# Performance work log

Hardware: AMD Instinct MI355X
Metric: run time of the kernel (lower is better)

The kernel has to match this reference:

```python
import jax, jax.numpy as jnp
import numpy as np

NI = 256        # in_channels
QK = NI // 8    # query/key channels = 32
BS, H, W = 4, 64, 64


def setup_inputs() -> dict:
    key = jax.random.key(0)
    ks = jax.random.split(key, 8)
    x = jax.random.normal(ks[0], (BS, NI, H, W), dtype=jnp.float32)
    # 1x1 conv weights stored as [out_ch, in_ch] (kernel is 1x1)
    wq = jax.random.normal(ks[1], (QK, NI), dtype=jnp.float32) * (1.0 / np.sqrt(NI))
    bq = jnp.zeros((QK,), dtype=jnp.float32)
    wk = jax.random.normal(ks[2], (QK, NI), dtype=jnp.float32) * (1.0 / np.sqrt(NI))
    bk = jnp.zeros((QK,), dtype=jnp.float32)
    wv = jax.random.normal(ks[3], (NI, NI), dtype=jnp.float32) * (1.0 / np.sqrt(NI))
    bv = jnp.zeros((NI,), dtype=jnp.float32)
    # gamma is zero-init in the module; use small random values so the
    # attention branch actually contributes (post-training state).
    gamma = jax.random.normal(ks[4], (1, NI, 1, 1), dtype=jnp.float32) * 0.1
    return {"x": x, "wq": wq, "bq": bq, "wk": wk, "bk": bk,
            "wv": wv, "bv": bv, "gamma": gamma}


def reference(x, wq, bq, wk, bk, wv, bv, gamma):
    bs, c, h, w = x.shape
    n = h * w
    xf = x.reshape(bs, c, n)                       # [bs, c, N]
    # 1x1 convs == per-pixel linear maps over channels
    q = jnp.einsum('oc,bcn->bno', wq, xf) + bq     # [bs, N, qk]
    k = jnp.einsum('oc,bcn->bon', wk, xf) + bk[None, :, None]  # [bs, qk, N]
    v = jnp.einsum('oc,bcn->bon', wv, xf) + bv[None, :, None]  # [bs, c, N]
    attn = jax.nn.softmax(jnp.einsum('bnq,bqm->bnm', q, k), axis=-1)  # [bs, N, N]
    out = jnp.einsum('bcm,bnm->bcn', v, attn)      # value @ attn^T
    out = out.reshape(bs, c, h, w)
    return gamma * out + x
```

## Files before the change

### kernel.cpp

```cpp
#include <hip/hip_runtime.h>
#include <cstdint>
#include <cstddef>

#define NI   256
#define QKC  32
#define BS   4
#define NPIX 4096
#define LOG2E 1.4426950408889634f

typedef __bf16 bf16x8 __attribute__((ext_vector_type(8)));
typedef __bf16 bf16x4 __attribute__((ext_vector_type(4)));
typedef float  f32x16 __attribute__((ext_vector_type(16)));

__device__ inline f32x16 zero16() {
    f32x16 z;
    #pragma unroll
    for (int i = 0; i < 16; ++i) z[i] = 0.f;
    return z;
}

__global__ __launch_bounds__(256) void wconv_pack(
    const float* __restrict__ wq, const float* __restrict__ wk,
    const float* __restrict__ wv, __bf16* __restrict__ wpk)
{
    int f = blockIdx.x * 256 + threadIdx.x;
    int otl = f >> 10, rem = f & 1023;
    int kk = rem >> 6, h = (rem >> 5) & 1, l31 = rem & 31;
    int och = otl * 32 + l31, c0 = kk * 16 + 8 * h;
    const float* src = och < 32 ? wq + och * NI + c0
                     : och < 64 ? wk + (och - 32) * NI + c0
                                : wv + (och - 64) * NI + c0;
    float4 x0 = *(const float4*)src;
    float4 x1 = *(const float4*)(src + 4);
    __align__(16) __bf16 o8[8] = {
        (__bf16)x0.x, (__bf16)x0.y, (__bf16)x0.z, (__bf16)x0.w,
        (__bf16)x1.x, (__bf16)x1.y, (__bf16)x1.z, (__bf16)x1.w};
    *(uint4*)(wpk + (size_t)f * 8) = *(const uint4*)o8;
}

__global__ __launch_bounds__(256) void qkv_mfma(
    const float* __restrict__ x, const __bf16* __restrict__ wpk,
    const float* __restrict__ bq, const float* __restrict__ bk,
    const float* __restrict__ bv,
    __bf16* __restrict__ qpk, __bf16* __restrict__ kpk, __bf16* __restrict__ vpk)
{
    __shared__ __align__(16) __bf16 xT[32][264];
    __shared__ float bls[320];

    const int t = threadIdx.x, w = t >> 6, lane = t & 63;
    const int l31 = lane & 31, h = lane >> 5;
    const int b = blockIdx.y, n0 = blockIdx.x * 32, kt = blockIdx.x;

    for (int i = t; i < 320; i += 256)
        bls[i] = i < 32 ? bq[i] : i < 64 ? bk[i - 32] : bv[i - 64];

    {
        int n4 = (t & 7) * 4, cb = (t >> 3) * 8;
        float4 xv[8];
        #pragma unroll
        for (int j = 0; j < 8; ++j)
            xv[j] = *(const float4*)(x + ((size_t)(b * NI) + cb + j) * NPIX + n0 + n4);
        #pragma unroll
        for (int i = 0; i < 4; ++i) {
            __align__(16) __bf16 r8[8];
            #pragma unroll
            for (int j = 0; j < 8; ++j) r8[j] = (__bf16)((&xv[j].x)[i]);
            *(uint4*)&xT[n4 + i][cb] = *(const uint4*)r8;
        }
    }
    __syncthreads();

    f32x16 acc[3] = {zero16(), zero16(), zero16()};
    #pragma unroll 4
    for (int kk = 0; kk < 16; ++kk) {
        bf16x8 xf = *(const bf16x8*)&xT[l31][kk * 16 + 8 * h];
        #pragma unroll
        for (int jj = 0; jj < 3; ++jj) {
            int otl = w + 4 * jj;
            if (otl < 10) {
                bf16x8 wf = *(const bf16x8*)(wpk + (size_t)((otl * 16 + kk) * 64 + 32 * h + l31) * 8);
                acc[jj] = __builtin_amdgcn_mfma_f32_32x32x16_bf16(wf, xf, acc[jj], 0, 0, 0);
            }
        }
    }
    __syncthreads();

    __bf16 (*vT)[264] = xT;
    #pragma unroll
    for (int jj = 0; jj < 3; ++jj) {
        int otl = w + 4 * jj;
        if (otl >= 2 && otl < 10) {
            #pragma unroll
            for (int qd = 0; qd < 4; ++qd) {
                int c0v = (otl - 2) * 32 + 8 * qd + 4 * h;
                __align__(8) __bf16 q4[4];
                #pragma unroll
                for (int i = 0; i < 4; ++i)
                    q4[i] = (__bf16)(acc[jj][4 * qd + i] + bls[64 + c0v + i]);
                *(uint2*)&vT[l31][c0v] = *(const uint2*)q4;
            }
        }
    }
    #pragma unroll
    for (int jj = 0; jj < 3; ++jj) {
        int otl = w + 4 * jj;
        if (otl == 0) {
            #pragma unroll
            for (int kc = 0; kc < 2; ++kc) {
                __align__(16) __bf16 hi8[8], lo8[8];
                #pragma unroll
                for (int j = 0; j < 8; ++j) {
                    int r = 8 * kc + j;
                    int och = (r & 3) + 8 * (r >> 2) + 4 * h;
                    float val = (acc[jj][r] + bls[och]) * LOG2E;
                    __bf16 hh = (__bf16)val;
                    hi8[j] = hh;
                    lo8[j] = (__bf16)(val - (float)hh);
                }
                size_t base = ((((size_t)(b * 128 + kt) * 2 + 0) * 2 + kc) * 2 + h) * 32 + l31;
                *(uint4*)(qpk + base * 8) = *(const uint4*)hi8;
                size_t basel = ((((size_t)(b * 128 + kt) * 2 + 1) * 2 + kc) * 2 + h) * 32 + l31;
                *(uint4*)(qpk + basel * 8) = *(const uint4*)lo8;
            }
        } else if (otl == 1) {
            #pragma unroll
            for (int kc = 0; kc < 2; ++kc) {
                __align__(16) __bf16 k8[8];
                #pragma unroll
                for (int j = 0; j < 8; ++j) {
                    int r = 8 * kc + j;
                    int och = (r & 3) + 8 * (r >> 2) + 4 * h;
                    k8[j] = (__bf16)(acc[jj][r] + bls[32 + och]);
                }
                size_t base = (((size_t)(b * 128 + kt) * 2 + kc) * 2 + h) * 32 + l31;
                *(uint4*)(kpk + base * 8) = *(const uint4*)k8;
            }
        }
    }
    __syncthreads();

    #pragma unroll
    for (int kc = 0; kc < 2; ++kc)
        #pragma unroll
        for (int hh = 0; hh < 2; ++hh) {
            __align__(16) __bf16 f8[8];
            #pragma unroll
            for (int j = 0; j < 8; ++j) f8[j] = vT[16 * kc + 8 * hh + j][t];
            size_t base = (((size_t)(b * 128 + kt) * 2 + kc) * 2 + hh) * 256 + t;
            *(uint4*)(vpk + base * 8) = *(const uint4*)f8;
        }
}

__global__ __launch_bounds__(256, 4) void attn_mfma(
    const __bf16* __restrict__ qpk, const __bf16* __restrict__ kpk,
    const __bf16* __restrict__ vpk,
    __bf16* __restrict__ Opart, float* __restrict__ dpart)
{
    constexpr int MT = 32;
    __shared__ __align__(16) __bf16 pt_s[2][64][72];
    __shared__ float dwave[4][32];

    const int t = threadIdx.x;
    const int b = blockIdx.z;
    const int ksp = blockIdx.y >> 1, cs = blockIdx.y & 1;
    const int n0 = blockIdx.x * 64;
    const int w = t >> 6, lane = t & 63, l31 = lane & 31, h = lane >> 5;
    const int sr = w & 1, sc = w >> 1;
    const int kt0 = ksp * 64;
    const int cbase = 128 * cs + 32 * w + l31;

    const int qt = 2 * blockIdx.x + sr;
    bf16x8 qf[2][2];
    #pragma unroll
    for (int hl = 0; hl < 2; ++hl)
        #pragma unroll
        for (int kc = 0; kc < 2; ++kc)
            qf[hl][kc] = *(const bf16x8*)(qpk +
                (((((size_t)(b * 128 + qt) * 2 + hl) * 2 + kc) * 2 + h) * 32 + l31) * 8);

    auto kload = [&](int ktile, int kc) {
        return *(const bf16x8*)(kpk +
            ((((size_t)(b * 128 + ktile) * 2 + kc) * 2 + h) * 32 + l31) * 8);
    };
    const __bf16* vbase = vpk +
        ((((size_t)(b * 128 + kt0) * 2) * 2 + h) * 256 + cbase) * 8;

    f32x16 a0 = zero16(), a1 = zero16();
    float dacc = 0.f;

    auto sblock = [&](bf16x8 kh0, bf16x8 kh1, int buf) {
        f32x16 s = zero16();
        __builtin_amdgcn_s_setprio(1);
        s = __builtin_amdgcn_mfma_f32_32x32x16_bf16(kh0, qf[0][0], s, 0, 0, 0);
        s = __builtin_amdgcn_mfma_f32_32x32x16_bf16(kh1, qf[0][1], s, 0, 0, 0);
        s = __builtin_amdgcn_mfma_f32_32x32x16_bf16(kh0, qf[1][0], s, 0, 0, 0);
        s = __builtin_amdgcn_mfma_f32_32x32x16_bf16(kh1, qf[1][1], s, 0, 0, 0);
        __builtin_amdgcn_s_setprio(0);
        #pragma unroll
        for (int qd = 0; qd < 4; ++qd) {
            __align__(8) __bf16 e4[4];
            #pragma unroll
            for (int i = 0; i < 4; ++i) {
                float e = __builtin_amdgcn_exp2f(s[4 * qd + i]);
                dacc += e;
                e4[i] = (__bf16)e;
            }
            *(uint2*)&pt_s[buf][32 * sr + l31][32 * sc + 8 * qd + 4 * h] = *(const uint2*)e4;
        }
    };

    bf16x8 kh0 = kload(kt0 + sc, 0), kh1 = kload(kt0 + sc, 1);
    sblock(kh0, kh1, 0);
    kh0 = kload(kt0 + 2 + sc, 0); kh1 = kload(kt0 + 2 + sc, 1);
    __syncthreads();

    for (int mt = 0; mt < MT; ++mt) {
        const int cur = mt & 1;

        bf16x8 vf[2][2];
        #pragma unroll
        for (int i = 0; i < 2; ++i)
            #pragma unroll
            for (int kc = 0; kc < 2; ++kc)
                vf[i][kc] = *(const bf16x8*)(vbase +
                    ((size_t)(2 * mt + i) * 2 + kc) * (2 * 256 * 8));

        if (mt < MT - 1) {
            bf16x8 k0 = kh0, k1 = kh1;
            if (mt < MT - 2) {
                kh0 = kload(kt0 + 2 * (mt + 2) + sc, 0);
                kh1 = kload(kt0 + 2 * (mt + 2) + sc, 1);
            }
            sblock(k0, k1, 1 - cur);
        }

        __builtin_amdgcn_s_setprio(1);
        #pragma unroll
        for (int i = 0; i < 2; ++i)
            #pragma unroll
            for (int kc = 0; kc < 2; ++kc) {
                int col = 32 * i + 16 * kc + 8 * h;
                bf16x8 pa0 = *(const bf16x8*)&pt_s[cur][l31][col];
                bf16x8 pa1 = *(const bf16x8*)&pt_s[cur][32 + l31][col];
                a0 = __builtin_amdgcn_mfma_f32_32x32x16_bf16(pa0, vf[i][kc], a0, 0, 0, 0);
                a1 = __builtin_amdgcn_mfma_f32_32x32x16_bf16(pa1, vf[i][kc], a1, 0, 0, 0);
            }
        __builtin_amdgcn_s_setprio(0);
        __syncthreads();
    }

    float dtot = dacc + __shfl_xor(dacc, 32);
    if (lane < 32) dwave[w][l31] = dtot;
    __syncthreads();
    if (cs == 0 && w < 2 && lane < 32) {
        size_t dbase = ((size_t)(ksp * BS + b)) * NPIX + n0 + 32 * w;
        dpart[dbase + l31] = dwave[w][l31] + dwave[w + 2][l31];
    }

    size_t obase = (((size_t)(ksp * BS + b)) * NI + cbase) * NPIX + n0;
    #pragma unroll
    for (int rq = 0; rq < 4; ++rq) {
        int nn = 8 * rq + 4 * h;
        __align__(8) __bf16 t0[4], t1[4];
        #pragma unroll
        for (int i = 0; i < 4; ++i) {
            t0[i] = (__bf16)a0[4 * rq + i];
            t1[i] = (__bf16)a1[4 * rq + i];
        }
        *(uint2*)(Opart + obase + nn)      = *(const uint2*)t0;
        *(uint2*)(Opart + obase + 32 + nn) = *(const uint2*)t1;
    }
}

__global__ __launch_bounds__(256) void combine(
    const float* __restrict__ x, const float* __restrict__ gamma,
    const __bf16* __restrict__ Opart, const float* __restrict__ dpart,
    float* __restrict__ out)
{
    int idx = (blockIdx.x * 256 + threadIdx.x) * 4;
    int n = idx & (NPIX - 1);
    int c = (idx >> 12) & (NI - 1);
    int b = idx >> 20;

    size_t o0 = (((size_t)(0 * BS + b)) * NI + c) * NPIX + n;
    size_t o1 = (((size_t)(1 * BS + b)) * NI + c) * NPIX + n;
    bf16x4 p0 = *(const bf16x4*)(Opart + o0);
    bf16x4 p1 = *(const bf16x4*)(Opart + o1);
    float4 da = *(const float4*)(dpart + ((size_t)(0 * BS + b)) * NPIX + n);
    float4 db = *(const float4*)(dpart + ((size_t)(1 * BS + b)) * NPIX + n);
    size_t xb = ((size_t)(b * NI) + c) * NPIX + n;
    float4 xv = *(const float4*)(x + xb);
    float g = gamma[c];

    float4 r;
    r.x = g * (((float)p0[0] + (float)p1[0]) / (da.x + db.x)) + xv.x;
    r.y = g * (((float)p0[1] + (float)p1[1]) / (da.y + db.y)) + xv.y;
    r.z = g * (((float)p0[2] + (float)p1[2]) / (da.z + db.z)) + xv.z;
    r.w = g * (((float)p0[3] + (float)p1[3]) / (da.w + db.w)) + xv.w;
    *(float4*)(out + xb) = r;
}

extern "C" void kernel_launch(void* const* d_in, const int* in_sizes, int n_in,
                              void* d_out, int out_size, void* d_ws, size_t ws_size,
                              hipStream_t stream)
{
    const float* x     = (const float*)d_in[0];
    const float* wq    = (const float*)d_in[1];
    const float* bq    = (const float*)d_in[2];
    const float* wk    = (const float*)d_in[3];
    const float* bk    = (const float*)d_in[4];
    const float* wv    = (const float*)d_in[5];
    const float* bv    = (const float*)d_in[6];
    const float* gamma = (const float*)d_in[7];
    float* out = (float*)d_out;

    const size_t WPK = (size_t)10240 * 8;
    const size_t QPK = (size_t)BS * 128 * 2 * 2 * 2 * 32 * 8;
    const size_t KPK = (size_t)BS * 128 * 2 * 2 * 32 * 8;
    const size_t VPK = (size_t)BS * 128 * 2 * 2 * 256 * 8;
    const size_t OSZ = (size_t)2 * BS * NI * NPIX;
    __bf16* wpk   = (__bf16*)d_ws;
    __bf16* qpk   = wpk + WPK;
    __bf16* kpk   = qpk + QPK;
    __bf16* vpk   = kpk + KPK;
    __bf16* Opart = vpk + VPK;
    float*  dpart = (float*)(Opart + OSZ);

    wconv_pack<<<dim3(40), 256, 0, stream>>>(wq, wk, wv, wpk);
    qkv_mfma<<<dim3(NPIX / 32, BS), 256, 0, stream>>>(x, wpk, bq, bk, bv, qpk, kpk, vpk);
    attn_mfma<<<dim3(64, 4, BS), 256, 0, stream>>>(qpk, kpk, vpk, Opart, dpart);
    combine<<<dim3(BS * NI * NPIX / 1024), 256, 0, stream>>>(x, gamma, Opart, dpart, out);
}
```

Measured before the change: 161.1 us.

## Merge channel splits into 512-thread attention blocks with 4-buffer swizzled P tile

```diff
diff --git a/kernel.cpp b/kernel.cpp
--- a/kernel.cpp
+++ b/kernel.cpp
@@ -151,25 +151,22 @@
         }
 }
 
-__global__ __launch_bounds__(256, 4) void attn_mfma(
+__global__ __launch_bounds__(512, 4) void attn_mfma(
     const __bf16* __restrict__ qpk, const __bf16* __restrict__ kpk,
     const __bf16* __restrict__ vpk,
     __bf16* __restrict__ Opart, float* __restrict__ dpart)
 {
-    constexpr int MT = 32;
-    __shared__ __align__(16) __bf16 pt_s[2][64][72];
-    __shared__ float dwave[4][32];
+    __shared__ __align__(16) __bf16 pt_s[4][64 * 64];
+    __shared__ float dwave[8][32];
 
     const int t = threadIdx.x;
-    const int b = blockIdx.z;
-    const int ksp = blockIdx.y >> 1, cs = blockIdx.y & 1;
-    const int n0 = blockIdx.x * 64;
+    const int b = blockIdx.x & 3, ksp = blockIdx.x >> 2;
+    const int n0 = blockIdx.y * 64;
     const int w = t >> 6, lane = t & 63, l31 = lane & 31, h = lane >> 5;
-    const int sr = w & 1, sc = w >> 1;
+    const int q = w & 3, sr = q & 1, sc = q >> 1, pp = w >> 2;
     const int kt0 = ksp * 64;
-    const int cbase = 128 * cs + 32 * w + l31;
-
-    const int qt = 2 * blockIdx.x + sr;
+
+    const int qt = 2 * blockIdx.y + sr;
     bf16x8 qf[2][2];
     #pragma unroll
     for (int hl = 0; hl < 2; ++hl)
@@ -182,8 +179,10 @@
         return *(const bf16x8*)(kpk +
             ((((size_t)(b * 128 + ktile) * 2 + kc) * 2 + h) * 32 + l31) * 8);
     };
-    const __bf16* vbase = vpk +
-        ((((size_t)(b * 128 + kt0) * 2) * 2 + h) * 256 + cbase) * 8;
+    auto vload = [&](int ktile, int kc) {
+        return *(const bf16x8*)(vpk +
+            ((((size_t)(b * 128 + ktile) * 2 + kc) * 2 + h) * 256 + 32 * w + l31) * 8);
+    };
 
     f32x16 a0 = zero16(), a1 = zero16();
     float dacc = 0.f;
@@ -196,6 +195,8 @@
         s = __builtin_amdgcn_mfma_f32_32x32x16_bf16(kh0, qf[1][0], s, 0, 0, 0);
         s = __builtin_amdgcn_mfma_f32_32x32x16_bf16(kh1, qf[1][1], s, 0, 0, 0);
         __builtin_amdgcn_s_setprio(0);
+        char* base = (char*)&pt_s[buf][0];
+        const int row = 32 * sr + l31;
         #pragma unroll
         for (int qd = 0; qd < 4; ++qd) {
             __align__(8) __bf16 e4[4];
@@ -205,59 +206,64 @@
                 dacc += e;
                 e4[i] = (__bf16)e;
             }
-            *(uint2*)&pt_s[buf][32 * sr + l31][32 * sc + 8 * qd + 4 * h] = *(const uint2*)e4;
-        }
-    };
-
-    bf16x8 kh0 = kload(kt0 + sc, 0), kh1 = kload(kt0 + sc, 1);
-    sblock(kh0, kh1, 0);
-    kh0 = kload(kt0 + 2 + sc, 0); kh1 = kload(kt0 + 2 + sc, 1);
-    __syncthreads();
-
-    for (int mt = 0; mt < MT; ++mt) {
-        const int cur = mt & 1;
-
-        bf16x8 vf[2][2];
+            int off = (64 * sc + 16 * qd + 8 * h) ^ ((row & 7) << 4);
+            *(uint2*)(base + row * 128 + off) = *(const uint2*)e4;
+        }
+    };
+
+    auto paread = [&](int buf, int nr, int i, int kc) {
+        const int row = 32 * nr + l31;
+        int off = (64 * i + 32 * kc + 16 * h) ^ ((row & 7) << 4);
+        return *(const bf16x8*)((const char*)&pt_s[buf][0] + row * 128 + off);
+    };
+
+    auto pvblock = [&](int m) {
+        const int buf = m & 3;
+        __builtin_amdgcn_s_setprio(1);
         #pragma unroll
         for (int i = 0; i < 2; ++i)
             #pragma unroll
-            for (int kc = 0; kc < 2; ++kc)
-                vf[i][kc] = *(const bf16x8*)(vbase +
-                    ((size_t)(2 * mt + i) * 2 + kc) * (2 * 256 * 8));
-
-        if (mt < MT - 1) {
+            for (int kc = 0; kc < 2; ++kc) {
+                bf16x8 vfik = vload(kt0 + 2 * m + i, kc);
+                bf16x8 pa0 = paread(buf, 0, i, kc);
+                bf16x8 pa1 = paread(buf, 1, i, kc);
+                a0 = __builtin_amdgcn_mfma_f32_32x32x16_bf16(pa0, vfik, a0, 0, 0, 0);
+                a1 = __builtin_amdgcn_mfma_f32_32x32x16_bf16(pa1, vfik, a1, 0, 0, 0);
+            }
+        __builtin_amdgcn_s_setprio(0);
+    };
+
+    bf16x8 kh0 = kload(kt0 + 2 * pp + sc, 0), kh1 = kload(kt0 + 2 * pp + sc, 1);
+    sblock(kh0, kh1, pp);
+    kh0 = kload(kt0 + 2 * (2 + pp) + sc, 0);
+    kh1 = kload(kt0 + 2 * (2 + pp) + sc, 1);
+    __syncthreads();
+
+    for (int j = 0; j < 16; ++j) {
+        if (j < 15) {
             bf16x8 k0 = kh0, k1 = kh1;
-            if (mt < MT - 2) {
-                kh0 = kload(kt0 + 2 * (mt + 2) + sc, 0);
-                kh1 = kload(kt0 + 2 * (mt + 2) + sc, 1);
-            }
-            sblock(k0, k1, 1 - cur);
-        }
-
-        __builtin_amdgcn_s_setprio(1);
-        #pragma unroll
-        for (int i = 0; i < 2; ++i)
-            #pragma unroll
-            for (int kc = 0; kc < 2; ++kc) {
-                int col = 32 * i + 16 * kc + 8 * h;
-                bf16x8 pa0 = *(const bf16x8*)&pt_s[cur][l31][col];
-                bf16x8 pa1 = *(const bf16x8*)&pt_s[cur][32 + l31][col];
-                a0 = __builtin_amdgcn_mfma_f32_32x32x16_bf16(pa0, vf[i][kc], a0, 0, 0, 0);
-                a1 = __builtin_amdgcn_mfma_f32_32x32x16_bf16(pa1, vf[i][kc], a1, 0, 0, 0);
-            }
-        __builtin_amdgcn_s_setprio(0);
+            if (j < 14) {
+                const int mtsn = 2 * j + 4 + pp;
+                kh0 = kload(kt0 + 2 * mtsn + sc, 0);
+                kh1 = kload(kt0 + 2 * mtsn + sc, 1);
+            }
+            sblock(k0, k1, (2 * j + 2 + pp) & 3);
+        }
+        pvblock(2 * j);
+        pvblock(2 * j + 1);
         __syncthreads();
     }
 
     float dtot = dacc + __shfl_xor(dacc, 32);
     if (lane < 32) dwave[w][l31] = dtot;
     __syncthreads();
-    if (cs == 0 && w < 2 && lane < 32) {
-        size_t dbase = ((size_t)(ksp * BS + b)) * NPIX + n0 + 32 * w;
-        dpart[dbase + l31] = dwave[w][l31] + dwave[w + 2][l31];
-    }
-
-    size_t obase = (((size_t)(ksp * BS + b)) * NI + cbase) * NPIX + n0;
+    if (w < 2 && lane < 32) {
+        float dsum = dwave[w][l31] + dwave[w + 2][l31]
+                   + dwave[w + 4][l31] + dwave[w + 6][l31];
+        dpart[((size_t)(ksp * BS + b)) * NPIX + n0 + 32 * w + l31] = dsum;
+    }
+
+    size_t obase = (((size_t)(ksp * BS + b)) * NI + 32 * w + l31) * NPIX + n0;
     #pragma unroll
     for (int rq = 0; rq < 4; ++rq) {
         int nn = 8 * rq + 4 * h;
@@ -328,6 +334,6 @@
 
     wconv_pack<<<dim3(40), 256, 0, stream>>>(wq, wk, wv, wpk);
     qkv_mfma<<<dim3(NPIX / 32, BS), 256, 0, stream>>>(x, wpk, bq, bk, bv, qpk, kpk, vpk);
-    attn_mfma<<<dim3(64, 4, BS), 256, 0, stream>>>(qpk, kpk, vpk, Opart, dpart);
+    attn_mfma<<<dim3(8, 64), 512, 0, stream>>>(qpk, kpk, vpk, Opart, dpart);
     combine<<<dim3(BS * NI * NPIX / 1024), 256, 0, stream>>>(x, gamma, Opart, dpart, out);
 }
```

Result: faster. 157.9 us (-2.0%).
